# Performance work log

Measured on AMD Instinct MI355X. Metric: run time of the kernel, lower is better.

## Reference

```python
import jax, jax.numpy as jnp
import numpy as np

EMBED_DIM = 2048
N_HEADS = 16
D_HEAD = EMBED_DIM // N_HEADS


def setup_inputs() -> dict:
    key = jax.random.key(0)
    kx, kq, kk, kv = jax.random.split(key, 4)
    B, N, D = 4, 2048, EMBED_DIM
    x = jax.random.normal(kx, (B, N, D), dtype=jnp.float32)
    Wq = jax.random.normal(kq, (D, D), dtype=jnp.float32) * 0.02
    Wk = jax.random.normal(kk, (D, D), dtype=jnp.float32) * 0.02
    Wv = jax.random.normal(kv, (D, D), dtype=jnp.float32) * 0.02
    return {"x": x, "Wq": Wq, "Wk": Wk, "Wv": Wv}


def reference(x, Wq, Wk, Wv):
    # x: [B, N, D]; weights applied as x @ W (matching torch.matmul in source)
    B, N, D = x.shape
    H, d = N_HEADS, D_HEAD
    # [B, N, D] -> [B, H, N, d]
    Q = (x @ Wq).reshape(B, N, H, d).transpose(0, 2, 1, 3)
    K = (x @ Wk).reshape(B, N, H, d).transpose(0, 2, 1, 3)
    V = (x @ Wv).reshape(B, N, H, d).transpose(0, 2, 1, 3)
    scale = 1.0 / jnp.sqrt(jnp.asarray(d, dtype=x.dtype))
    # non-causal SDPA (torch default: no mask, scale = 1/sqrt(d_head))
    scores = jnp.einsum('bhqd,bhkd->bhqk', Q, K) * scale  # [B,H,N,N]
    attn = jax.nn.softmax(scores, axis=-1)
    out = jnp.einsum('bhqk,bhkd->bhqd', attn, V)  # [B,H,N,d]
    return out
```

## Files before the change

### kernel.cpp

```cpp
#include <hip/hip_runtime.h>
#include <hip/hip_bf16.h>

#define B 4
#define N 2048
#define D 2048
#define H 16
#define DH 128
#define NT 32

typedef unsigned short u16;
typedef __attribute__((ext_vector_type(8))) short short8;
typedef __attribute__((ext_vector_type(4))) float floatx4;

__device__ __forceinline__ u16 f2b(float f) {
    union { __hip_bfloat16 h; u16 u; } cv;
    cv.h = __float2bfloat16(f);
    return cv.u;
}

__device__ __forceinline__ floatx4 mfma16(short8 a, short8 b, floatx4 c) {
    return __builtin_amdgcn_mfma_f32_16x16x32_bf16(a, b, c, 0, 0, 0);
}

#if __has_builtin(__builtin_amdgcn_exp2f)
#define EXP2(x) __builtin_amdgcn_exp2f(x)
#else
#define EXP2(x) exp2f(x)
#endif

__device__ __forceinline__ void async16(const void* g, void* l) {
    __builtin_amdgcn_global_load_lds(
        (const __attribute__((address_space(1))) unsigned int*)g,
        (__attribute__((address_space(3))) unsigned int*)l, 16, 0, 0);
}

__global__ __launch_bounds__(256) void cvt_x(const float* __restrict__ x,
                                             u16* __restrict__ xb) {
    size_t i = ((size_t)blockIdx.x * 256 + threadIdx.x) * 8;
    float4 v0 = *(const float4*)&x[i];
    float4 v1 = *(const float4*)&x[i + 4];
    union { u16 u[8]; uint4 s; } pk;
    pk.u[0] = f2b(v0.x); pk.u[1] = f2b(v0.y); pk.u[2] = f2b(v0.z); pk.u[3] = f2b(v0.w);
    pk.u[4] = f2b(v1.x); pk.u[5] = f2b(v1.y); pk.u[6] = f2b(v1.z); pk.u[7] = f2b(v1.w);
    *(uint4*)&xb[i] = pk.s;
}

__global__ __launch_bounds__(256) void cvt_w_t(const float* __restrict__ Wq,
                                               const float* __restrict__ Wk,
                                               const float* __restrict__ Wv,
                                               u16* __restrict__ wt) {
    __shared__ float tile[64][65];
    const int z = blockIdx.z;
    const float* W = (z == 0) ? Wq : (z == 1) ? Wk : Wv;
    const float scl = (z == 0) ? 0.12751743342f : 1.0f;
    const int k0 = blockIdx.x * 64, n0 = blockIdx.y * 64;
    const int tr = threadIdx.x >> 4, tc = threadIdx.x & 15;
#pragma unroll
    for (int i = 0; i < 4; i++) {
        int kk = tr + 16 * i;
        float4 vv = *(const float4*)&W[(size_t)(k0 + kk) * D + n0 + tc * 4];
        tile[kk][tc * 4 + 0] = vv.x; tile[kk][tc * 4 + 1] = vv.y;
        tile[kk][tc * 4 + 2] = vv.z; tile[kk][tc * 4 + 3] = vv.w;
    }
    __syncthreads();
#pragma unroll
    for (int i = 0; i < 4; i++) {
        int nn = tr + 16 * i;
        union { u16 u[4]; ushort4 s; } pk;
#pragma unroll
        for (int j = 0; j < 4; j++) pk.u[j] = f2b(tile[tc * 4 + j][nn] * scl);
        *(ushort4*)&wt[(size_t)z * D * D + (size_t)(n0 + nn) * D + k0 + tc * 4] = pk.s;
    }
}

#define KT 32
#define SGB __builtin_amdgcn_sched_group_barrier
__global__ __launch_bounds__(512, 2) void qkv_gemm(const u16* __restrict__ xb,
                                                   const u16* __restrict__ wt,
                                                   u16* __restrict__ qo,
                                                   u16* __restrict__ ko,
                                                   u16* __restrict__ vo) {
    __shared__ u16 lds[81920];

    const int bid = blockIdx.x;
    const int c = bid & 7, i = bid >> 3;
    const int i6 = (i * 43) >> 8;
    const int tm = ((c >> 2) << 4) + i6;
    const int tn = (c & 3) * 6 + (i - 6 * i6);

    const int t = threadIdx.x, lane = t & 63, w = t >> 6;
    const int wr = w >> 2, wc = w & 3;
    const int q4 = lane >> 4, lr = lane & 15;

    const int m0 = tm * 256;
    const int n0 = tn * 256;

    unsigned aoff[2][2], boff[2][2];
#pragma unroll
    for (int ii = 0; ii < 2; ii++) {
        const int off = ii * 8192 + w * 1024 + lane * 16;
        const int row = off >> 7;
        const int s = (off >> 4) & 7;
        const int col = ((s ^ (row & 7))) * 8;
#pragma unroll
        for (int h = 0; h < 2; h++) {
            aoff[h][ii] = (unsigned)((m0 + h * 128 + row) * D + col);
            boff[h][ii] = (unsigned)((n0 + h * 128 + row) * D + col);
        }
    }

    const unsigned cb0 = (unsigned)(((0 * 4 + q4) ^ (lr & 7)) * 16);
    const unsigned cb1 = (unsigned)(((1 * 4 + q4) ^ (lr & 7)) * 16);
    const unsigned aC0 = (unsigned)(wr * 16384 + lr * 128) + cb0;
    const unsigned aC1 = (unsigned)(wr * 16384 + lr * 128) + cb1;
    const unsigned bC0 = (unsigned)((wc >> 1) * 16384 + (wc & 1) * 8192 + lr * 128) + cb0;
    const unsigned bC1 = (unsigned)((wc >> 1) * 16384 + (wc & 1) * 8192 + lr * 128) + cb1;

#define STAGE_A(bufoff, h, j) {                                                           \
    async16(xb + aoff[h][0] + (unsigned)(j) * 64,                                         \
            (char*)lds + (bufoff) + (h) * 16384 + w * 1024);                              \
    async16(xb + aoff[h][1] + (unsigned)(j) * 64,                                         \
            (char*)lds + (bufoff) + (h) * 16384 + 8192 + w * 1024); }
#define STAGE_B(bufoff, h, j) {                                                           \
    async16(wt + boff[h][0] + (unsigned)(j) * 64,                                         \
            (char*)lds + (bufoff) + (h) * 16384 + w * 1024);                              \
    async16(wt + boff[h][1] + (unsigned)(j) * 64,                                         \
            (char*)lds + (bufoff) + (h) * 16384 + 8192 + w * 1024); }
#define BAR() __builtin_amdgcn_s_barrier()
#define DSR(off) (*(const short8*)((const char*)lds + (off)))

    floatx4 acc[8][4];
#pragma unroll
    for (int x = 0; x < 8; x++)
#pragma unroll
        for (int j = 0; j < 4; j++) acc[x][j] = (floatx4){0.f, 0.f, 0.f, 0.f};

    STAGE_A(0u, 0, 0); STAGE_A(0u, 1, 0);
    STAGE_B(98304u, 0, 0); STAGE_B(98304u, 1, 0);
    STAGE_A(32768u, 0, 1); STAGE_A(32768u, 1, 1);
    asm volatile("s_waitcnt vmcnt(4)" ::: "memory");
    BAR();

    unsigned aOffR = 0u;
    unsigned aOffW = 65536u;

    for (int g = 0; g < KT; g++) {
        const unsigned bR = 98304u + (unsigned)((g & 1) << 15);
        const unsigned bW = 98304u + (unsigned)(((g + 1) & 1) << 15);

        if (g + 1 < KT) { STAGE_B(bW, 0, g + 1); STAGE_B(bW, 1, g + 1); }
        if (g + 2 < KT) { STAGE_A(aOffW, 0, g + 2); STAGE_A(aOffW, 1, g + 2); }
        __builtin_amdgcn_sched_barrier(0);

        const unsigned aB0 = aOffR + aC0, aB1 = aOffR + aC1;
        const unsigned bB0 = bR + bC0, bB1 = bR + bC1;

        short8 a0k0[4], a0k1[4], a1k0[4], a1k1[4];
        short8 b0k0[2], b0k1[2], b1k0[2], b1k1[2];

        b0k0[0] = DSR(bB0);        b0k0[1] = DSR(bB0 + 2048);
#pragma unroll
        for (int mf = 0; mf < 4; mf++) a0k0[mf] = DSR(aB0 + mf * 2048);
#pragma unroll
        for (int mf = 0; mf < 4; mf++) a1k0[mf] = DSR(aB0 + 8192 + mf * 2048);
#pragma unroll
        for (int nf = 0; nf < 2; nf++)
#pragma unroll
            for (int mf = 0; mf < 4; mf++)
                acc[mf][nf] = mfma16(a0k0[mf], b0k0[nf], acc[mf][nf]);
        b1k0[0] = DSR(bB0 + 4096); b1k0[1] = DSR(bB0 + 6144);
#pragma unroll
        for (int nf = 0; nf < 2; nf++)
#pragma unroll
            for (int mf = 0; mf < 4; mf++)
                acc[4 + mf][nf] = mfma16(a1k0[mf], b0k0[nf], acc[4 + mf][nf]);
        b0k1[0] = DSR(bB1);        b0k1[1] = DSR(bB1 + 2048);
#pragma unroll
        for (int mf = 0; mf < 4; mf++) a0k1[mf] = DSR(aB1 + mf * 2048);
#pragma unroll
        for (int nf = 0; nf < 2; nf++)
#pragma unroll
            for (int mf = 0; mf < 4; mf++)
                acc[4 + mf][2 + nf] = mfma16(a1k0[mf], b1k0[nf], acc[4 + mf][2 + nf]);
#pragma unroll
        for (int mf = 0; mf < 4; mf++) a1k1[mf] = DSR(aB1 + 8192 + mf * 2048);
#pragma unroll
        for (int nf = 0; nf < 2; nf++)
#pragma unroll
            for (int mf = 0; mf < 4; mf++)
                acc[mf][2 + nf] = mfma16(a0k0[mf], b1k0[nf], acc[mf][2 + nf]);
        b1k1[0] = DSR(bB1 + 4096); b1k1[1] = DSR(bB1 + 6144);
#pragma unroll
        for (int nf = 0; nf < 2; nf++)
#pragma unroll
            for (int mf = 0; mf < 4; mf++)
                acc[mf][nf] = mfma16(a0k1[mf], b0k1[nf], acc[mf][nf]);
#pragma unroll
        for (int nf = 0; nf < 2; nf++)
#pragma unroll
            for (int mf = 0; mf < 4; mf++)
                acc[4 + mf][nf] = mfma16(a1k1[mf], b0k1[nf], acc[4 + mf][nf]);
#pragma unroll
        for (int nf = 0; nf < 2; nf++)
#pragma unroll
            for (int mf = 0; mf < 4; mf++)
                acc[4 + mf][2 + nf] = mfma16(a1k1[mf], b1k1[nf], acc[4 + mf][2 + nf]);
#pragma unroll
        for (int nf = 0; nf < 2; nf++)
#pragma unroll
            for (int mf = 0; mf < 4; mf++)
                acc[mf][2 + nf] = mfma16(a0k1[mf], b1k1[nf], acc[mf][2 + nf]);

        SGB(0x100, 10, 0);
        SGB(0x008,  8, 0);
        SGB(0x100,  2, 0);
        SGB(0x008,  8, 0);
        SGB(0x100,  6, 0);
        SGB(0x008,  8, 0);
        SGB(0x100,  4, 0);
        SGB(0x008,  8, 0);
        SGB(0x100,  2, 0);
        SGB(0x008,  8, 0);
        SGB(0x008,  8, 0);
        SGB(0x008,  8, 0);
        SGB(0x008,  8, 0);

        if (g == KT - 2) { asm volatile("s_waitcnt vmcnt(0)" ::: "memory"); }
        else if (g < KT - 2) { asm volatile("s_waitcnt vmcnt(4)" ::: "memory"); }
        if (g + 1 < KT) BAR();

        aOffR = (aOffR == 65536u) ? 0u : aOffR + 32768u;
        aOffW = (aOffW == 65536u) ? 0u : aOffW + 32768u;
    }

    const int z = tn >> 3;
    u16* dst = (z == 0) ? qo : (z == 1) ? ko : vo;
    const int c2b = (tn & 7) * 256 + wc * 64;
    const int grb = tm * 256 + wr * 128;
#pragma unroll
    for (int mf = 0; mf < 8; mf++)
#pragma unroll
        for (int nf = 0; nf < 4; nf++)
#pragma unroll
            for (int r = 0; r < 4; r++) {
                int gr = grb + mf * 16 + q4 * 4 + r;
                int c2 = c2b + nf * 16 + lr;
                int b_ = gr >> 11, n_ = gr & (N - 1);
                int head = c2 >> 7, dcol = c2 & 127;
                dst[((size_t)(b_ * H + head) * N + n_) * DH + dcol] = f2b(acc[mf][nf][r]);
            }
#undef STAGE_A
#undef STAGE_B
#undef BAR
#undef DSR
}

__global__ __launch_bounds__(256) void transpose_v(const u16* __restrict__ v,
                                                   u16* __restrict__ vt) {
    __shared__ u16 tile[64][72];
    const int bh = blockIdx.z;
    const int n0 = blockIdx.x * 64, d0 = blockIdx.y * 64;
    const int t = threadIdx.x;
#pragma unroll
    for (int i = 0; i < 2; i++) {
        int gid = t + 256 * i;
        int nl = gid >> 3, g = gid & 7;
        *(uint4*)&tile[nl][g * 8] =
            *(const uint4*)&v[((size_t)bh * N + n0 + nl) * DH + d0 + g * 8];
    }
    __syncthreads();
#pragma unroll
    for (int i = 0; i < 2; i++) {
        int gid = t + 256 * i;
        int dl = gid >> 3, gn = gid & 7;
        union { u16 u[8]; uint4 s; } pk;
#pragma unroll
        for (int j = 0; j < 8; j++) {
            int kp = gn * 8 + j;
            int src = 32 * (kp >> 5) + 16 * ((kp >> 2) & 1) + 4 * ((kp >> 3) & 3) + (kp & 3);
            pk.u[j] = tile[src][dl];
        }
        *(uint4*)&vt[((size_t)bh * DH + d0 + dl) * N + n0 + gn * 8] = pk.s;
    }
}

#define FMAX2 17.312340491f
__global__ __launch_bounds__(256, 2) void attn_kernel(const u16* __restrict__ q,
                                                      const u16* __restrict__ k,
                                                      const u16* __restrict__ vt,
                                                      float* __restrict__ out) {
    __shared__ __align__(16) char smem[66560];

    const int beta = blockIdx.x;
    const int bh = (beta & 7) + 8 * (beta >> 7);
    const int qt = (beta >> 3) & 15;
    const int t = threadIdx.x;
    const int w = t >> 6, lane = t & 63;
    const int q4 = lane >> 4, lr = lane & 15;
    const int a = w & 1, b = w >> 1;

    const size_t qbase = ((size_t)bh * N + (size_t)qt * 128) * DH;
    short8 af[4][4];
#pragma unroll
    for (int rt = 0; rt < 4; rt++)
#pragma unroll
        for (int ks = 0; ks < 4; ks++)
            af[rt][ks] = *(const short8*)&q[qbase + (size_t)(64 * b + 16 * rt + lr) * DH
                                            + ks * 32 + q4 * 8];

    float lrow[4] = {0.f, 0.f, 0.f, 0.f};
    floatx4 o[4][8];
#pragma unroll
    for (int rt = 0; rt < 4; rt++)
#pragma unroll
        for (int cv = 0; cv < 8; cv++) o[rt][cv] = (floatx4){0.f, 0.f, 0.f, 0.f};

    const u16* kpB = k + (size_t)bh * N * DH;
    const u16* vpB = vt + (size_t)bh * DH * N;
    unsigned koff[4], voff[4];
#pragma unroll
    for (int c = 0; c < 4; c++) {
        int grp = 4 * w + c;
        int krow = 4 * grp + (lane >> 4);
        int kg = (lane & 15) ^ (krow & 15);
        koff[c] = (unsigned)(krow * DH + kg * 8);
        int vrow = 8 * grp + (lane >> 3);
        int vg = (lane & 7) ^ (vrow & 7);
        voff[c] = (unsigned)(vrow * N + vg * 8);
    }

    unsigned kaddr[4];
#pragma unroll
    for (int ks = 0; ks < 4; ks++)
        kaddr[ks] = (unsigned)((32 * a + lr) * 256 + (((4 * ks + q4) ^ lr) * 16));
    unsigned vaddr = (unsigned)(32768 + lr * 128 + (((4 * a + q4) ^ (lr & 7)) * 16));

#pragma unroll
    for (int c = 0; c < 4; c++) {
        async16(kpB + koff[c], smem + (4 * w + c) * 1024);
        async16(vpB + voff[c], smem + 32768 + (4 * w + c) * 1024);
    }

    for (int kt = 0; kt < NT; kt++) {
        __syncthreads();

        if (kt + 1 < NT) {
            const int nb = (kt + 1) & 1;
#pragma unroll
            for (int c = 0; c < 4; c++) {
                async16(kpB + koff[c] + (unsigned)(kt + 1) * 64 * DH,
                        smem + nb * 16384 + (4 * w + c) * 1024);
                async16(vpB + voff[c] + (unsigned)(kt + 1) * 64,
                        smem + 32768 + nb * 16384 + (4 * w + c) * 1024);
            }
        }

        unsigned paw[4][4];
        {
            short8 bf[4];
#pragma unroll
            for (int ks = 0; ks < 4; ks++)
                bf[ks] = *(const short8*)(smem + kaddr[ks]);
#pragma unroll
            for (int rt = 0; rt < 4; rt++) {
                floatx4 s = (floatx4){0.f, 0.f, 0.f, 0.f};
#pragma unroll
                for (int ks = 0; ks < 4; ks++) s = mfma16(bf[ks], af[rt][ks], s);
                float p0 = EXP2(s[0] - FMAX2), p1 = EXP2(s[1] - FMAX2);
                float p2 = EXP2(s[2] - FMAX2), p3 = EXP2(s[3] - FMAX2);
                lrow[rt] += (p0 + p1) + (p2 + p3);
                paw[rt][0] = (unsigned)f2b(p0) | ((unsigned)f2b(p1) << 16);
                paw[rt][1] = (unsigned)f2b(p2) | ((unsigned)f2b(p3) << 16);
            }
#pragma unroll
            for (int ks = 0; ks < 4; ks++)
                bf[ks] = *(const short8*)(smem + kaddr[ks] + 4096);
#pragma unroll
            for (int rt = 0; rt < 4; rt++) {
                floatx4 s = (floatx4){0.f, 0.f, 0.f, 0.f};
#pragma unroll
                for (int ks = 0; ks < 4; ks++) s = mfma16(bf[ks], af[rt][ks], s);
                float p0 = EXP2(s[0] - FMAX2), p1 = EXP2(s[1] - FMAX2);
                float p2 = EXP2(s[2] - FMAX2), p3 = EXP2(s[3] - FMAX2);
                lrow[rt] += (p0 + p1) + (p2 + p3);
                paw[rt][2] = (unsigned)f2b(p0) | ((unsigned)f2b(p1) << 16);
                paw[rt][3] = (unsigned)f2b(p2) | ((unsigned)f2b(p3) << 16);
            }
        }
        short8 PA[4];
#pragma unroll
        for (int rt = 0; rt < 4; rt++) {
            union { unsigned uu[4]; short8 s8; } cv_;
            cv_.uu[0] = paw[rt][0]; cv_.uu[1] = paw[rt][1];
            cv_.uu[2] = paw[rt][2]; cv_.uu[3] = paw[rt][3];
            PA[rt] = cv_.s8;
        }

#pragma unroll
        for (int ctv = 0; ctv < 8; ctv++) {
            short8 bv = *(const short8*)(smem + vaddr + ctv * 2048);
#pragma unroll
            for (int rt = 0; rt < 4; rt++)
                o[rt][ctv] = mfma16(PA[rt], bv, o[rt][ctv]);
        }

#pragma unroll
        for (int ks = 0; ks < 4; ks++) kaddr[ks] ^= 16384u;
        vaddr ^= 16384u;
    }

    __syncthreads();
    float* Ls = (float*)smem;
#pragma unroll
    for (int rt = 0; rt < 4; rt++) {
        float s = lrow[rt];
        s += __shfl_xor(s, 16);
        s += __shfl_xor(s, 32);
        if (q4 == 0) Ls[a * 128 + 64 * b + 16 * rt + lr] = s;
    }
    __syncthreads();

    floatx4 inv4[4];
#pragma unroll
    for (int rt = 0; rt < 4; rt++)
#pragma unroll
        for (int r = 0; r < 4; r++) {
            int row = 64 * b + 16 * rt + 4 * q4 + r;
            inv4[rt][r] = 1.f / (Ls[row] + Ls[128 + row]);
        }

    char* Ox = smem + 1024;
    if (a == 1) {
#pragma unroll
        for (int rt = 0; rt < 4; rt++)
#pragma unroll
            for (int ctv = 0; ctv < 8; ctv++) {
                int dd = 16 * ctv + lr;
                int slot = (16 * b + 4 * rt + q4) ^ (dd & 31);
                floatx4 v = o[rt][ctv];
                v[0] *= inv4[rt][0]; v[1] *= inv4[rt][1];
                v[2] *= inv4[rt][2]; v[3] *= inv4[rt][3];
                *(floatx4*)(Ox + dd * 512 + slot * 16) = v;
            }
    }
    __syncthreads();
    if (a == 0) {
        const size_t obase = ((size_t)bh * N + (size_t)qt * 128) * DH;
#pragma unroll
        for (int rt = 0; rt < 4; rt++)
#pragma unroll
            for (int ctv = 0; ctv < 8; ctv++) {
                int dd = 16 * ctv + lr;
                int slot = (16 * b + 4 * rt + q4) ^ (dd & 31);
                floatx4 vx = *(const floatx4*)(Ox + dd * 512 + slot * 16);
#pragma unroll
                for (int r = 0; r < 4; r++) {
                    int row = 64 * b + 16 * rt + 4 * q4 + r;
                    out[obase + (size_t)row * DH + dd] =
                        o[rt][ctv][r] * inv4[rt][r] + vx[r];
                }
            }
    }
}

extern "C" void kernel_launch(void* const* d_in, const int* in_sizes, int n_in,
                              void* d_out, int out_size, void* d_ws, size_t ws_size,
                              hipStream_t stream) {
    const float* x  = (const float*)d_in[0];
    const float* Wq = (const float*)d_in[1];
    const float* Wk = (const float*)d_in[2];
    const float* Wv = (const float*)d_in[3];
    float* out = (float*)d_out;
    char* ws = (char*)d_ws;

    u16* xb = (u16*)(ws);
    u16* wt = (u16*)(ws + 33554432);
    u16* qb = (u16*)(ws + 58720256);
    u16* kb = (u16*)(ws + 92274688);
    u16* vb = (u16*)(ws + 125829120);
    u16* vtb = (u16*)(ws);

    cvt_x<<<dim3(8192), dim3(256), 0, stream>>>(x, xb);
    cvt_w_t<<<dim3(32, 32, 3), dim3(256), 0, stream>>>(Wq, Wk, Wv, wt);
    qkv_gemm<<<dim3(768), dim3(512), 0, stream>>>(xb, wt, qb, kb, vb);
    transpose_v<<<dim3(32, 2, 64), dim3(256), 0, stream>>>(vb, vtb);
    attn_kernel<<<dim3(1024), dim3(256), 0, stream>>>(qb, kb, vtb, out);
}
```

Before: 543.6 us.

## Split attention work by query rows per warp instead of key halves

Each of the four warps now owns 32 query rows and processes all 64 keys of every tile, instead of a 2x2 split of query rows and key halves. This removes the final cross-warp reduction of partial outputs and row sums through shared memory, along with a barrier. It also halves the per-warp output accumulator and Q fragment registers. In exchange, each warp reads twice as many K and V fragments from LDS per tile, which raises shared-memory traffic.

```diff
diff --git a/kernel.cpp b/kernel.cpp
--- a/kernel.cpp
+++ b/kernel.cpp
@@ -289,7 +289,7 @@
                                                       const u16* __restrict__ k,
                                                       const u16* __restrict__ vt,
                                                       float* __restrict__ out) {
-    __shared__ __align__(16) char smem[66560];
+    __shared__ __align__(16) char smem[65536];
 
     const int beta = blockIdx.x;
     const int bh = (beta & 7) + 8 * (beta >> 7);
@@ -297,21 +297,20 @@
     const int t = threadIdx.x;
     const int w = t >> 6, lane = t & 63;
     const int q4 = lane >> 4, lr = lane & 15;
-    const int a = w & 1, b = w >> 1;
 
     const size_t qbase = ((size_t)bh * N + (size_t)qt * 128) * DH;
-    short8 af[4][4];
-#pragma unroll
-    for (int rt = 0; rt < 4; rt++)
+    short8 af[2][4];
+#pragma unroll
+    for (int rt = 0; rt < 2; rt++)
 #pragma unroll
         for (int ks = 0; ks < 4; ks++)
-            af[rt][ks] = *(const short8*)&q[qbase + (size_t)(64 * b + 16 * rt + lr) * DH
+            af[rt][ks] = *(const short8*)&q[qbase + (size_t)(32 * w + 16 * rt + lr) * DH
                                             + ks * 32 + q4 * 8];
 
-    float lrow[4] = {0.f, 0.f, 0.f, 0.f};
-    floatx4 o[4][8];
-#pragma unroll
-    for (int rt = 0; rt < 4; rt++)
+    float lrow[2] = {0.f, 0.f};
+    floatx4 o[2][8];
+#pragma unroll
+    for (int rt = 0; rt < 2; rt++)
 #pragma unroll
         for (int cv = 0; cv < 8; cv++) o[rt][cv] = (floatx4){0.f, 0.f, 0.f, 0.f};
 
@@ -332,8 +331,11 @@
     unsigned kaddr[4];
 #pragma unroll
     for (int ks = 0; ks < 4; ks++)
-        kaddr[ks] = (unsigned)((32 * a + lr) * 256 + (((4 * ks + q4) ^ lr) * 16));
-    unsigned vaddr = (unsigned)(32768 + lr * 128 + (((4 * a + q4) ^ (lr & 7)) * 16));
+        kaddr[ks] = (unsigned)(lr * 256 + (((4 * ks + q4) ^ lr) * 16));
+    unsigned vaddr[2];
+#pragma unroll
+    for (int a = 0; a < 2; a++)
+        vaddr[a] = (unsigned)(32768 + lr * 128 + (((4 * a + q4) ^ (lr & 7)) * 16));
 
 #pragma unroll
     for (int c = 0; c < 4; c++) {
@@ -355,111 +357,77 @@
             }
         }
 
-        unsigned paw[4][4];
-        {
+        unsigned paw[2][4][2];
+#pragma unroll
+        for (int ct = 0; ct < 4; ct++) {
             short8 bf[4];
 #pragma unroll
             for (int ks = 0; ks < 4; ks++)
-                bf[ks] = *(const short8*)(smem + kaddr[ks]);
-#pragma unroll
-            for (int rt = 0; rt < 4; rt++) {
+                bf[ks] = *(const short8*)(smem + kaddr[ks] + ct * 4096);
+#pragma unroll
+            for (int rt = 0; rt < 2; rt++) {
                 floatx4 s = (floatx4){0.f, 0.f, 0.f, 0.f};
 #pragma unroll
                 for (int ks = 0; ks < 4; ks++) s = mfma16(bf[ks], af[rt][ks], s);
                 float p0 = EXP2(s[0] - FMAX2), p1 = EXP2(s[1] - FMAX2);
                 float p2 = EXP2(s[2] - FMAX2), p3 = EXP2(s[3] - FMAX2);
                 lrow[rt] += (p0 + p1) + (p2 + p3);
-                paw[rt][0] = (unsigned)f2b(p0) | ((unsigned)f2b(p1) << 16);
-                paw[rt][1] = (unsigned)f2b(p2) | ((unsigned)f2b(p3) << 16);
-            }
-#pragma unroll
-            for (int ks = 0; ks < 4; ks++)
-                bf[ks] = *(const short8*)(smem + kaddr[ks] + 4096);
-#pragma unroll
-            for (int rt = 0; rt < 4; rt++) {
-                floatx4 s = (floatx4){0.f, 0.f, 0.f, 0.f};
-#pragma unroll
-                for (int ks = 0; ks < 4; ks++) s = mfma16(bf[ks], af[rt][ks], s);
-                float p0 = EXP2(s[0] - FMAX2), p1 = EXP2(s[1] - FMAX2);
-                float p2 = EXP2(s[2] - FMAX2), p3 = EXP2(s[3] - FMAX2);
-                lrow[rt] += (p0 + p1) + (p2 + p3);
-                paw[rt][2] = (unsigned)f2b(p0) | ((unsigned)f2b(p1) << 16);
-                paw[rt][3] = (unsigned)f2b(p2) | ((unsigned)f2b(p3) << 16);
-            }
-        }
-        short8 PA[4];
-#pragma unroll
-        for (int rt = 0; rt < 4; rt++) {
-            union { unsigned uu[4]; short8 s8; } cv_;
-            cv_.uu[0] = paw[rt][0]; cv_.uu[1] = paw[rt][1];
-            cv_.uu[2] = paw[rt][2]; cv_.uu[3] = paw[rt][3];
-            PA[rt] = cv_.s8;
-        }
+                paw[rt][ct][0] = (unsigned)f2b(p0) | ((unsigned)f2b(p1) << 16);
+                paw[rt][ct][1] = (unsigned)f2b(p2) | ((unsigned)f2b(p3) << 16);
+            }
+        }
+        short8 PA[2][2];
+#pragma unroll
+        for (int rt = 0; rt < 2; rt++)
+#pragma unroll
+            for (int a = 0; a < 2; a++) {
+                union { unsigned uu[4]; short8 s8; } cv_;
+                cv_.uu[0] = paw[rt][2 * a][0];     cv_.uu[1] = paw[rt][2 * a][1];
+                cv_.uu[2] = paw[rt][2 * a + 1][0]; cv_.uu[3] = paw[rt][2 * a + 1][1];
+                PA[rt][a] = cv_.s8;
+            }
 
 #pragma unroll
         for (int ctv = 0; ctv < 8; ctv++) {
-            short8 bv = *(const short8*)(smem + vaddr + ctv * 2048);
-#pragma unroll
-            for (int rt = 0; rt < 4; rt++)
-                o[rt][ctv] = mfma16(PA[rt], bv, o[rt][ctv]);
+#pragma unroll
+            for (int a = 0; a < 2; a++) {
+                short8 bv = *(const short8*)(smem + vaddr[a] + ctv * 2048);
+#pragma unroll
+                for (int rt = 0; rt < 2; rt++)
+                    o[rt][ctv] = mfma16(PA[rt][a], bv, o[rt][ctv]);
+            }
         }
 
 #pragma unroll
         for (int ks = 0; ks < 4; ks++) kaddr[ks] ^= 16384u;
-        vaddr ^= 16384u;
-    }
-
-    __syncthreads();
+        vaddr[0] ^= 16384u; vaddr[1] ^= 16384u;
+    }
+
     float* Ls = (float*)smem;
 #pragma unroll
-    for (int rt = 0; rt < 4; rt++) {
+    for (int rt = 0; rt < 2; rt++) {
         float s = lrow[rt];
         s += __shfl_xor(s, 16);
         s += __shfl_xor(s, 32);
-        if (q4 == 0) Ls[a * 128 + 64 * b + 16 * rt + lr] = s;
+        if (q4 == 0) Ls[32 * w + 16 * rt + lr] = s;
     }
     __syncthreads();
-
-    floatx4 inv4[4];
-#pragma unroll
-    for (int rt = 0; rt < 4; rt++)
-#pragma unroll
-        for (int r = 0; r < 4; r++) {
-            int row = 64 * b + 16 * rt + 4 * q4 + r;
-            inv4[rt][r] = 1.f / (Ls[row] + Ls[128 + row]);
-        }
-
-    char* Ox = smem + 1024;
-    if (a == 1) {
-#pragma unroll
-        for (int rt = 0; rt < 4; rt++)
-#pragma unroll
-            for (int ctv = 0; ctv < 8; ctv++) {
-                int dd = 16 * ctv + lr;
-                int slot = (16 * b + 4 * rt + q4) ^ (dd & 31);
-                floatx4 v = o[rt][ctv];
-                v[0] *= inv4[rt][0]; v[1] *= inv4[rt][1];
-                v[2] *= inv4[rt][2]; v[3] *= inv4[rt][3];
-                *(floatx4*)(Ox + dd * 512 + slot * 16) = v;
-            }
-    }
-    __syncthreads();
-    if (a == 0) {
-        const size_t obase = ((size_t)bh * N + (size_t)qt * 128) * DH;
-#pragma unroll
-        for (int rt = 0; rt < 4; rt++)
-#pragma unroll
-            for (int ctv = 0; ctv < 8; ctv++) {
-                int dd = 16 * ctv + lr;
-                int slot = (16 * b + 4 * rt + q4) ^ (dd & 31);
-                floatx4 vx = *(const floatx4*)(Ox + dd * 512 + slot * 16);
-#pragma unroll
-                for (int r = 0; r < 4; r++) {
-                    int row = 64 * b + 16 * rt + 4 * q4 + r;
-                    out[obase + (size_t)row * DH + dd] =
-                        o[rt][ctv][r] * inv4[rt][r] + vx[r];
-                }
-            }
+    const size_t obase = ((size_t)bh * N + (size_t)qt * 128) * DH;
+#pragma unroll
+    for (int rt = 0; rt < 2; rt++) {
+        floatx4 inv4;
+#pragma unroll
+        for (int r = 0; r < 4; r++)
+            inv4[r] = 1.f / Ls[32 * w + 16 * rt + 4 * q4 + r];
+#pragma unroll
+        for (int ctv = 0; ctv < 8; ctv++) {
+            int dd = 16 * ctv + lr;
+#pragma unroll
+            for (int r = 0; r < 4; r++) {
+                int row = 32 * w + 16 * rt + 4 * q4 + r;
+                out[obase + (size_t)row * DH + dd] = o[rt][ctv][r] * inv4[r];
+            }
+        }
     }
 }
 
```

New measurement: 466.0 us. 1.17x faster.
